# Optimization experiments

Hardware: AMD Instinct MI355X
Metric: run time of the kernel (lower is better)

## Reference

```python
import jax, jax.numpy as jnp
import numpy as np

N_FILTERS = 100
WINDOWS = (2, 3, 4, 5)
B, S, W, D = 64, 400, 16, 64
VOCAB, HID = 96, 128


def setup_inputs() -> dict:
    key = jax.random.key(0)
    ks = jax.random.split(key, 16)
    inp = {
        'char_idxs': jax.random.randint(ks[0], (B, S, W), 0, VOCAB),
        'char_vectors': jax.random.normal(ks[1], (VOCAB, D), jnp.float32),
        'filt2': jax.random.normal(ks[2], (N_FILTERS, 2 * D), jnp.float32) * 0.05,
        'filt3': jax.random.normal(ks[3], (N_FILTERS, 3 * D), jnp.float32) * 0.05,
        'filt4': jax.random.normal(ks[4], (N_FILTERS, 4 * D), jnp.float32) * 0.05,
        'filt5': jax.random.normal(ks[5], (N_FILTERS, 5 * D), jnp.float32) * 0.05,
        'w_proj': jax.random.normal(ks[6], (HID, 4 * N_FILTERS), jnp.float32) * 0.05,
        't_w0': jax.random.normal(ks[7], (HID, HID), jnp.float32) * 0.05,
        't_b0': jax.random.normal(ks[8], (HID,), jnp.float32) * 0.05,
        't_w1': jax.random.normal(ks[9], (HID, HID), jnp.float32) * 0.05,
        't_b1': jax.random.normal(ks[10], (HID,), jnp.float32) * 0.05,
        'g_w0': jax.random.normal(ks[11], (HID, HID), jnp.float32) * 0.05,
        'g_b0': jax.random.normal(ks[12], (HID,), jnp.float32) * 0.05,
        'g_w1': jax.random.normal(ks[13], (HID, HID), jnp.float32) * 0.05,
        'g_b1': jax.random.normal(ks[14], (HID,), jnp.float32) * 0.05,
    }
    return inp


def _conv_branch(embed, filt, w):
    # embed: [B, S, W, D]; filt: [100, w*D]
    b, s, wl, d = embed.shape
    L = wl - w + 1  # valid positions
    idx = jnp.arange(L)[:, None] + jnp.arange(w)  # [L, w]
    xw = embed[:, :, idx, :].reshape(b, s, L, w * d)  # [B,S,L,w*D]
    h = jnp.tanh(jnp.einsum('bslk,fk->bslf', xw, filt))  # [B,S,L,100]
    return h.max(axis=2)  # max-pool over all positions -> [B,S,100]


def reference(char_idxs, char_vectors, filt2, filt3, filt4, filt5, w_proj,
              t_w0, t_b0, t_w1, t_b1, g_w0, g_b0, g_w1, g_b1):
    embed = char_vectors[char_idxs]  # [B,S,W,D]
    outs = jnp.concatenate(
        [_conv_branch(embed, f, w) for f, w in zip((filt2, filt3, filt4, filt5), WINDOWS)],
        axis=-1)  # [B,S,400]
    x = outs @ w_proj.T  # no-bias linear -> [B,S,HID]
    # 2-layer highway: x = g*relu(Wt x + bt) + (1-g)*x, g = sigmoid(Wg x + bg)
    for tw, tb, gw, gb in ((t_w0, t_b0, g_w0, g_b0), (t_w1, t_b1, g_w1, g_b1)):
        g = jax.nn.sigmoid(x @ gw.T + gb)
        t = jax.nn.relu(x @ tw.T + tb)
        x = g * t + (1.0 - g) * x
    return x
```

## Files before the change

### kernel.cpp

```cpp
#include <hip/hip_runtime.h>

#define NT     25600
#define WCH    16
#define DIM    64
#define VOCAB  96
#define HID    128
#define KP     416
#define TOKB   64

typedef __attribute__((ext_vector_type(8))) _Float16 h8;
typedef __attribute__((ext_vector_type(4))) float f32x4;

__device__ __forceinline__ float tanh_fast(float m) {
  float t = fminf(fmaxf(m, -9.f), 9.f);
  float e = __builtin_amdgcn_exp2f(t * 2.885390082f);
  return 1.f - 2.f * __builtin_amdgcn_rcpf(e + 1.f);
}

__global__ __launch_bounds__(256) void k_prep(
    const float* __restrict__ cv,
    const float* __restrict__ f2, const float* __restrict__ f3,
    const float* __restrict__ f4, const float* __restrict__ f5,
    const float* __restrict__ wproj,
    const float* __restrict__ tw0, const float* __restrict__ gw0,
    const float* __restrict__ tw1, const float* __restrict__ gw1,
    _Float16* __restrict__ T2, _Float16* __restrict__ wprojP,
    _Float16* __restrict__ hw) {
  __shared__ float fS[100 * 65];
  __shared__ float cvS[8 * 65];
  const int tid = threadIdx.x;
  const int b = blockIdx.x;

  if (b < 168) {
    const int slot = b / 12, cg = b - slot * 12;
    int wi, j;
    if (slot < 2)      { wi = 0; j = slot; }
    else if (slot < 5) { wi = 1; j = slot - 2; }
    else if (slot < 9) { wi = 2; j = slot - 5; }
    else               { wi = 3; j = slot - 9; }
    const float* filt = (wi == 0) ? f2 : (wi == 1) ? f3 : (wi == 2) ? f4 : f5;
    const int rowlen = (wi + 2) * DIM;
    for (int idx = tid; idx < 100 * DIM; idx += 256) {
      int f = idx >> 6, d = idx & 63;
      fS[f * 65 + d] = filt[f * rowlen + j * DIM + d];
    }
    for (int idx = tid; idx < 8 * DIM; idx += 256) {
      int c = idx >> 6, d = idx & 63;
      cvS[c * 65 + d] = cv[(cg * 8 + c) * DIM + d];
    }
    __syncthreads();
    for (int idx = tid; idx < 8 * 104; idx += 256) {
      int cl = idx / 104, f = idx - cl * 104;
      float s = 0.f;
      if (f < 100) {
#pragma unroll 8
        for (int d = 0; d < DIM; ++d) s += cvS[cl * 65 + d] * fS[f * 65 + d];
      }
      T2[((size_t)(f >> 3) * 14 + slot) * 768 + (cg * 8 + cl) * 8 + (f & 7)] =
          (_Float16)s;
    }
  } else if (b < 232) {
    const int n = (b - 168) * 2 + (tid >> 7);
    for (int k = tid & 127; k < KP; k += 128) {
      int s8 = k >> 3;
      int wi = s8 / 13;
      int fl = (s8 - wi * 13) * 8 + (k & 7);
      wprojP[n * KP + k] =
          (fl < 100) ? (_Float16)wproj[n * 400 + wi * 100 + fl] : (_Float16)0.f;
    }
  } else {
    const int idx = (b - 232) * 256 + tid;
    const int which = idx >> 14, r = idx & 16383;
    const float* src = (which == 0) ? tw0 : (which == 1) ? gw0
                     : (which == 2) ? tw1 : gw1;
    hw[idx] = (_Float16)src[r];
  }
}

template<int WI>
__device__ __forceinline__ void conv_oct(const _Float16* __restrict__ Ts,
                                         const int* __restrict__ ch,
                                         _Float16* __restrict__ convA,
                                         int token, int o) {
  constexpr int W = WI + 2, L = 15 - WI;
  constexpr int SB = (WI == 0) ? 0 : (WI == 1) ? 2 : (WI == 2) ? 5 : 9;
  h8 m;
  {
    h8 s = *(const h8*)(Ts + SB * 768 + ch[0]);
#pragma unroll
    for (int j = 1; j < W; ++j) s += *(const h8*)(Ts + (SB + j) * 768 + ch[j]);
    m = s;
  }
#pragma unroll
  for (int l = 1; l < L; ++l) {
    h8 s = *(const h8*)(Ts + SB * 768 + ch[l]);
#pragma unroll
    for (int j = 1; j < W; ++j) s += *(const h8*)(Ts + (SB + j) * 768 + ch[l + j]);
    m = __builtin_elementwise_max(m, s);
  }
  h8 r;
#pragma unroll
  for (int i = 0; i < 8; ++i) r[i] = (_Float16)tanh_fast((float)m[i]);
  const int s8 = WI * 13 + o;
  *(h8*)(convA + (s8 * 64 + (token & 48) + ((token & 15) ^ (s8 & 15))) * 8) = r;
}

__global__ __launch_bounds__(256) void k_fused(
    const int* __restrict__ chars,
    const _Float16* __restrict__ T2,
    const _Float16* __restrict__ wprojP,
    const _Float16* __restrict__ hw,
    const float* __restrict__ tb0, const float* __restrict__ tb1,
    const float* __restrict__ gb0, const float* __restrict__ gb1,
    float* __restrict__ out) {
  __shared__ __align__(16) char lds[78848];
  _Float16* Ts    = (_Float16*)lds;
  _Float16* xA    = (_Float16*)lds;
  _Float16* convA = (_Float16*)(lds + 21504);
  int*      chS   = (int*)(lds + 21504 + 53248);

  const int tid = threadIdx.x;
  const int wave = tid >> 6, lane = tid & 63;
  const int m16 = lane & 15, quad = lane >> 4;
  const int tok0 = blockIdx.x * TOKB;
  const f32x4 zero = {0.f, 0.f, 0.f, 0.f};

#pragma unroll
  for (int k = 0; k < 4; ++k) {
    int idx = tid + k * 256;
    int t = idx >> 4, i = idx & 15;
    chS[i * 64 + t] = chars[(tok0 + t) * WCH + i] * 8;
  }
  __syncthreads();

  const int token = tid & 63;
  int ch[WCH];
#pragma unroll
  for (int i = 0; i < WCH; ++i) ch[i] = chS[i * 64 + token];

  for (int o = 0; o < 13; ++o) {
    if (o) __syncthreads();
    const _Float16* src = T2 + (size_t)o * 10752;
    for (int r = tid; r < 1344; r += 256)
      *(h8*)(Ts + r * 8) = *(const h8*)(src + r * 8);
    __syncthreads();
    switch ((wave + o) & 3) {
      case 0: conv_oct<0>(Ts, ch, convA, token, o); break;
      case 1: conv_oct<1>(Ts, ch, convA, token, o); break;
      case 2: conv_oct<2>(Ts, ch, convA, token, o); break;
      default: conv_oct<3>(Ts, ch, convA, token, o); break;
    }
  }
  __syncthreads();

  const int hcA = wave * 16 + m16;
  const int hcB = hcA + 64;
  f32x4 xp[4][2];
#pragma unroll
  for (int mt = 0; mt < 4; ++mt) { xp[mt][0] = zero; xp[mt][1] = zero; }

  for (int ks = 0; ks < 13; ++ks) {
    const int s8 = ks * 4 + quad;
    h8 b0 = *(const h8*)(wprojP + (size_t)hcA * KP + s8 * 8);
    h8 b1 = *(const h8*)(wprojP + (size_t)hcB * KP + s8 * 8);
#pragma unroll
    for (int mt = 0; mt < 4; ++mt) {
      h8 a = *(const h8*)(convA + (s8 * 64 + mt * 16 + (m16 ^ (s8 & 15))) * 8);
      xp[mt][0] = __builtin_amdgcn_mfma_f32_16x16x32_f16(a, b0, xp[mt][0], 0, 0, 0);
      xp[mt][1] = __builtin_amdgcn_mfma_f32_16x16x32_f16(a, b1, xp[mt][1], 0, 0, 0);
    }
  }

#pragma unroll
  for (int mt = 0; mt < 4; ++mt)
#pragma unroll
    for (int nt = 0; nt < 2; ++nt) {
      int col = nt * 64 + hcA;
#pragma unroll
      for (int r = 0; r < 4; ++r)
        xA[(col >> 3) * 512 + (mt * 16 + quad * 4 + r) * 8 + (col & 7)] =
            (_Float16)xp[mt][nt][r];
    }
  __syncthreads();

#pragma unroll
  for (int layer = 0; layer < 2; ++layer) {
    const _Float16* tw = hw + (layer ? 2 : 0) * HID * HID;
    const _Float16* gw = hw + (layer ? 3 : 1) * HID * HID;
    const float* tbv = layer ? tb1 : tb0;
    const float* gbv = layer ? gb1 : gb0;
    float btA = tbv[hcA], bgA = gbv[hcA];
    float btB = tbv[hcB], bgB = gbv[hcB];

    f32x4 at[4][2], ag[4][2];
#pragma unroll
    for (int mt = 0; mt < 4; ++mt) {
      at[mt][0] = zero; at[mt][1] = zero;
      ag[mt][0] = zero; ag[mt][1] = zero;
    }
#pragma unroll
    for (int ks = 0; ks < 4; ++ks) {
      const int ko = ks * 32 + quad * 8;
      h8 bt0 = *(const h8*)(tw + (size_t)hcA * HID + ko);
      h8 bt1 = *(const h8*)(tw + (size_t)hcB * HID + ko);
      h8 bg0 = *(const h8*)(gw + (size_t)hcA * HID + ko);
      h8 bg1 = *(const h8*)(gw + (size_t)hcB * HID + ko);
#pragma unroll
      for (int mt = 0; mt < 4; ++mt) {
        h8 a = *(const h8*)(xA + (ks * 4 + quad) * 512 + (mt * 16 + m16) * 8);
        at[mt][0] = __builtin_amdgcn_mfma_f32_16x16x32_f16(a, bt0, at[mt][0], 0, 0, 0);
        at[mt][1] = __builtin_amdgcn_mfma_f32_16x16x32_f16(a, bt1, at[mt][1], 0, 0, 0);
        ag[mt][0] = __builtin_amdgcn_mfma_f32_16x16x32_f16(a, bg0, ag[mt][0], 0, 0, 0);
        ag[mt][1] = __builtin_amdgcn_mfma_f32_16x16x32_f16(a, bg1, ag[mt][1], 0, 0, 0);
      }
    }
    __syncthreads();

#pragma unroll
    for (int mt = 0; mt < 4; ++mt)
#pragma unroll
      for (int nt = 0; nt < 2; ++nt) {
        float bt = nt ? btB : btA, bg = nt ? bgB : bgA;
        int col = nt * 64 + hcA;
#pragma unroll
        for (int r = 0; r < 4; ++r) {
          float g = 1.f / (1.f + __builtin_amdgcn_exp2f(
                               -(ag[mt][nt][r] + bg) * 1.442695041f));
          float tt = fmaxf(at[mt][nt][r] + bt, 0.f);
          float xn = g * tt + (1.f - g) * xp[mt][nt][r];
          xp[mt][nt][r] = xn;
          int row = mt * 16 + quad * 4 + r;
          if (layer == 0)
            xA[(col >> 3) * 512 + row * 8 + (col & 7)] = (_Float16)xn;
          else
            out[(size_t)(tok0 + row) * HID + col] = xn;
        }
      }
    if (layer == 0) __syncthreads();
  }
}

extern "C" void kernel_launch(void* const* d_in, const int* in_sizes, int n_in,
                              void* d_out, int out_size, void* d_ws, size_t ws_size,
                              hipStream_t stream) {
  (void)in_sizes; (void)n_in; (void)out_size; (void)ws_size;
  const int* chars = (const int*)d_in[0];
  const float* cv  = (const float*)d_in[1];
  const float* f2  = (const float*)d_in[2];
  const float* f3  = (const float*)d_in[3];
  const float* f4  = (const float*)d_in[4];
  const float* f5  = (const float*)d_in[5];
  const float* wpj = (const float*)d_in[6];
  const float* tw0 = (const float*)d_in[7];
  const float* tb0 = (const float*)d_in[8];
  const float* tw1 = (const float*)d_in[9];
  const float* tb1 = (const float*)d_in[10];
  const float* gw0 = (const float*)d_in[11];
  const float* gb0 = (const float*)d_in[12];
  const float* gw1 = (const float*)d_in[13];
  const float* gb1 = (const float*)d_in[14];
  float* out = (float*)d_out;

  char* ws = (char*)d_ws;
  _Float16* T2     = (_Float16*)ws;
  _Float16* wprojP = (_Float16*)(ws + 279552);
  _Float16* hw     = (_Float16*)(ws + 279552 + 106496);

  k_prep<<<488, 256, 0, stream>>>(cv, f2, f3, f4, f5, wpj, tw0, gw0, tw1, gw1,
                                  T2, wprojP, hw);
  k_fused<<<NT / TOKB, 256, 0, stream>>>(chars, T2, wprojP, hw,
                                         tb0, tb1, gb0, gb1, out);
}
```

Before: 175.4 us.

## Split conv-to-projection into two passes to shrink LDS and raise occupancy

The 13 conv octets are processed in two passes (7 then 6). The projection MFMA accumulation runs after each pass, so the convA staging buffer only needs room for 28 groups instead of 52. The char-index LDS staging is replaced with direct vectorized global loads per lane, and the XOR swizzle on convA is dropped. LDS per block falls from about 77KB to 49KB, which should allow more resident blocks per CU. The cost is extra barriers, and the unswizzled convA layout may bring back LDS bank conflicts.

```diff
diff --git a/kernel.cpp b/kernel.cpp
--- a/kernel.cpp
+++ b/kernel.cpp
@@ -10,6 +10,7 @@
 
 typedef __attribute__((ext_vector_type(8))) _Float16 h8;
 typedef __attribute__((ext_vector_type(4))) float f32x4;
+typedef __attribute__((ext_vector_type(4))) int i32x4;
 
 __device__ __forceinline__ float tanh_fast(float m) {
   float t = fminf(fmaxf(m, -9.f), 9.f);
@@ -81,7 +82,7 @@
 __device__ __forceinline__ void conv_oct(const _Float16* __restrict__ Ts,
                                          const int* __restrict__ ch,
                                          _Float16* __restrict__ convA,
-                                         int token, int o) {
+                                         int lane, int ls8) {
   constexpr int W = WI + 2, L = 15 - WI;
   constexpr int SB = (WI == 0) ? 0 : (WI == 1) ? 2 : (WI == 2) ? 5 : 9;
   h8 m;
@@ -101,8 +102,7 @@
   h8 r;
 #pragma unroll
   for (int i = 0; i < 8; ++i) r[i] = (_Float16)tanh_fast((float)m[i]);
-  const int s8 = WI * 13 + o;
-  *(h8*)(convA + (s8 * 64 + (token & 48) + ((token & 15) ^ (s8 & 15))) * 8) = r;
+  *(h8*)(convA + (ls8 * 64 + lane) * 8) = r;
 }
 
 __global__ __launch_bounds__(256) void k_fused(
@@ -113,11 +113,10 @@
     const float* __restrict__ tb0, const float* __restrict__ tb1,
     const float* __restrict__ gb0, const float* __restrict__ gb1,
     float* __restrict__ out) {
-  __shared__ __align__(16) char lds[78848];
+  __shared__ __align__(16) char lds[50176];
   _Float16* Ts    = (_Float16*)lds;
   _Float16* xA    = (_Float16*)lds;
   _Float16* convA = (_Float16*)(lds + 21504);
-  int*      chS   = (int*)(lds + 21504 + 53248);
 
   const int tid = threadIdx.x;
   const int wave = tid >> 6, lane = tid & 63;
@@ -125,33 +124,16 @@
   const int tok0 = blockIdx.x * TOKB;
   const f32x4 zero = {0.f, 0.f, 0.f, 0.f};
 
-#pragma unroll
-  for (int k = 0; k < 4; ++k) {
-    int idx = tid + k * 256;
-    int t = idx >> 4, i = idx & 15;
-    chS[i * 64 + t] = chars[(tok0 + t) * WCH + i] * 8;
-  }
-  __syncthreads();
-
-  const int token = tid & 63;
   int ch[WCH];
-#pragma unroll
-  for (int i = 0; i < WCH; ++i) ch[i] = chS[i * 64 + token];
-
-  for (int o = 0; o < 13; ++o) {
-    if (o) __syncthreads();
-    const _Float16* src = T2 + (size_t)o * 10752;
-    for (int r = tid; r < 1344; r += 256)
-      *(h8*)(Ts + r * 8) = *(const h8*)(src + r * 8);
-    __syncthreads();
-    switch ((wave + o) & 3) {
-      case 0: conv_oct<0>(Ts, ch, convA, token, o); break;
-      case 1: conv_oct<1>(Ts, ch, convA, token, o); break;
-      case 2: conv_oct<2>(Ts, ch, convA, token, o); break;
-      default: conv_oct<3>(Ts, ch, convA, token, o); break;
-    }
-  }
-  __syncthreads();
+  {
+    const i32x4* cp = (const i32x4*)(chars + (size_t)(tok0 + lane) * WCH);
+#pragma unroll
+    for (int q = 0; q < 4; ++q) {
+      i32x4 v = cp[q];
+#pragma unroll
+      for (int i = 0; i < 4; ++i) ch[q * 4 + i] = v[i] * 8;
+    }
+  }
 
   const int hcA = wave * 16 + m16;
   const int hcB = hcA + 64;
@@ -159,18 +141,44 @@
 #pragma unroll
   for (int mt = 0; mt < 4; ++mt) { xp[mt][0] = zero; xp[mt][1] = zero; }
 
-  for (int ks = 0; ks < 13; ++ks) {
-    const int s8 = ks * 4 + quad;
-    h8 b0 = *(const h8*)(wprojP + (size_t)hcA * KP + s8 * 8);
-    h8 b1 = *(const h8*)(wprojP + (size_t)hcB * KP + s8 * 8);
-#pragma unroll
-    for (int mt = 0; mt < 4; ++mt) {
-      h8 a = *(const h8*)(convA + (s8 * 64 + mt * 16 + (m16 ^ (s8 & 15))) * 8);
-      xp[mt][0] = __builtin_amdgcn_mfma_f32_16x16x32_f16(a, b0, xp[mt][0], 0, 0, 0);
-      xp[mt][1] = __builtin_amdgcn_mfma_f32_16x16x32_f16(a, b1, xp[mt][1], 0, 0, 0);
-    }
-  }
-
+#pragma unroll
+  for (int pass = 0; pass < 2; ++pass) {
+    const int obeg = pass ? 7 : 0, oend = pass ? 13 : 7;
+    for (int o = obeg; o < oend; ++o) {
+      __syncthreads();
+      const _Float16* src = T2 + (size_t)o * 10752;
+      for (int r = tid; r < 1344; r += 256)
+        *(h8*)(Ts + r * 8) = *(const h8*)(src + r * 8);
+      __syncthreads();
+      const int win = (wave + o) & 3;
+      const int ls8 = pass ? (win * 6 + o - 7) : (win * 7 + o);
+      switch (win) {
+        case 0: conv_oct<0>(Ts, ch, convA, lane, ls8); break;
+        case 1: conv_oct<1>(Ts, ch, convA, lane, ls8); break;
+        case 2: conv_oct<2>(Ts, ch, convA, lane, ls8); break;
+        default: conv_oct<3>(Ts, ch, convA, lane, ls8); break;
+      }
+    }
+    __syncthreads();
+    const int ng = pass ? 6 : 7;
+    const int per = pass ? 6 : 7;
+    const int ob = pass ? 7 : 0;
+    for (int ks = 0; ks < ng; ++ks) {
+      const int g = ks * 4 + quad;
+      const int win = g / per;
+      const int s8 = win * 13 + (g - win * per) + ob;
+      h8 b0 = *(const h8*)(wprojP + (size_t)hcA * KP + s8 * 8);
+      h8 b1 = *(const h8*)(wprojP + (size_t)hcB * KP + s8 * 8);
+#pragma unroll
+      for (int mt = 0; mt < 4; ++mt) {
+        h8 a = *(const h8*)(convA + (g * 64 + mt * 16 + m16) * 8);
+        xp[mt][0] = __builtin_amdgcn_mfma_f32_16x16x32_f16(a, b0, xp[mt][0], 0, 0, 0);
+        xp[mt][1] = __builtin_amdgcn_mfma_f32_16x16x32_f16(a, b1, xp[mt][1], 0, 0, 0);
+      }
+    }
+  }
+
+  __syncthreads();
 #pragma unroll
   for (int mt = 0; mt < 4; ++mt)
 #pragma unroll
```

Result: no change. 178.7 us (+1.9%).

## Read conv tables from global directly, widen block to 8 waves

Applied to the files above, without the earlier changes.

Removes the per-octet staging of the conv lookup tables into LDS, along with its 13 block-wide barriers. Each wave now gathers straight from the global/L2-resident table, and a static load-balanced split of filter octets is spread across 8 waves instead of 4. The projection and highway GEMMs are repartitioned so each wave owns 16 output columns, and char indices are read with vector loads. LDS use drops, which may raise occupancy. The cost is that the scattered gathers now hit the cache hierarchy instead of LDS, and the convA swizzle is removed, which could introduce bank conflicts.

```diff
diff --git a/kernel.cpp b/kernel.cpp
--- a/kernel.cpp
+++ b/kernel.cpp
@@ -10,6 +10,7 @@
 
 typedef __attribute__((ext_vector_type(8))) _Float16 h8;
 typedef __attribute__((ext_vector_type(4))) float f32x4;
+typedef __attribute__((ext_vector_type(4))) int i32x4;
 
 __device__ __forceinline__ float tanh_fast(float m) {
   float t = fminf(fmaxf(m, -9.f), 9.f);
@@ -78,34 +79,35 @@
 }
 
 template<int WI>
-__device__ __forceinline__ void conv_oct(const _Float16* __restrict__ Ts,
-                                         const int* __restrict__ ch,
-                                         _Float16* __restrict__ convA,
-                                         int token, int o) {
+__device__ __forceinline__ void conv_g(const _Float16* __restrict__ T2,
+                                       const int* __restrict__ ch,
+                                       _Float16* __restrict__ convA,
+                                       int lane, int o) {
   constexpr int W = WI + 2, L = 15 - WI;
   constexpr int SB = (WI == 0) ? 0 : (WI == 1) ? 2 : (WI == 2) ? 5 : 9;
+  const _Float16* Tb = T2 + ((size_t)o * 14 + SB) * 768;
   h8 m;
   {
-    h8 s = *(const h8*)(Ts + SB * 768 + ch[0]);
-#pragma unroll
-    for (int j = 1; j < W; ++j) s += *(const h8*)(Ts + (SB + j) * 768 + ch[j]);
+    h8 s = *(const h8*)(Tb + ch[0]);
+#pragma unroll
+    for (int j = 1; j < W; ++j) s += *(const h8*)(Tb + j * 768 + ch[j]);
     m = s;
   }
 #pragma unroll
   for (int l = 1; l < L; ++l) {
-    h8 s = *(const h8*)(Ts + SB * 768 + ch[l]);
-#pragma unroll
-    for (int j = 1; j < W; ++j) s += *(const h8*)(Ts + (SB + j) * 768 + ch[l + j]);
+    h8 s = *(const h8*)(Tb + ch[l]);
+#pragma unroll
+    for (int j = 1; j < W; ++j) s += *(const h8*)(Tb + j * 768 + ch[l + j]);
     m = __builtin_elementwise_max(m, s);
   }
   h8 r;
 #pragma unroll
   for (int i = 0; i < 8; ++i) r[i] = (_Float16)tanh_fast((float)m[i]);
   const int s8 = WI * 13 + o;
-  *(h8*)(convA + (s8 * 64 + (token & 48) + ((token & 15) ^ (s8 & 15))) * 8) = r;
-}
-
-__global__ __launch_bounds__(256) void k_fused(
+  *(h8*)(convA + (s8 * 64 + lane) * 8) = r;
+}
+
+__global__ __launch_bounds__(512) void k_fused(
     const int* __restrict__ chars,
     const _Float16* __restrict__ T2,
     const _Float16* __restrict__ wprojP,
@@ -113,11 +115,9 @@
     const float* __restrict__ tb0, const float* __restrict__ tb1,
     const float* __restrict__ gb0, const float* __restrict__ gb1,
     float* __restrict__ out) {
-  __shared__ __align__(16) char lds[78848];
-  _Float16* Ts    = (_Float16*)lds;
+  __shared__ __align__(16) char lds[53248];
+  _Float16* convA = (_Float16*)lds;
   _Float16* xA    = (_Float16*)lds;
-  _Float16* convA = (_Float16*)(lds + 21504);
-  int*      chS   = (int*)(lds + 21504 + 53248);
 
   const int tid = threadIdx.x;
   const int wave = tid >> 6, lane = tid & 63;
@@ -125,62 +125,54 @@
   const int tok0 = blockIdx.x * TOKB;
   const f32x4 zero = {0.f, 0.f, 0.f, 0.f};
 
-#pragma unroll
-  for (int k = 0; k < 4; ++k) {
-    int idx = tid + k * 256;
-    int t = idx >> 4, i = idx & 15;
-    chS[i * 64 + t] = chars[(tok0 + t) * WCH + i] * 8;
+  int ch[WCH];
+  {
+    const i32x4* cp = (const i32x4*)(chars + (size_t)(tok0 + lane) * WCH);
+#pragma unroll
+    for (int q = 0; q < 4; ++q) {
+      i32x4 v = cp[q];
+#pragma unroll
+      for (int i = 0; i < 4; ++i) ch[q * 4 + i] = v[i] * 8;
+    }
+  }
+
+  switch (wave) {
+    case 0: for (int o = 0;  o < 5;  ++o) conv_g<3>(T2, ch, convA, lane, o); break;
+    case 1: for (int o = 5;  o < 10; ++o) conv_g<3>(T2, ch, convA, lane, o); break;
+    case 2: for (int o = 10; o < 13; ++o) conv_g<3>(T2, ch, convA, lane, o);
+            for (int o = 0;  o < 2;  ++o) conv_g<2>(T2, ch, convA, lane, o); break;
+    case 3: for (int o = 2;  o < 8;  ++o) conv_g<2>(T2, ch, convA, lane, o); break;
+    case 4: for (int o = 8;  o < 13; ++o) conv_g<2>(T2, ch, convA, lane, o);
+            conv_g<0>(T2, ch, convA, lane, 0); break;
+    case 5: for (int o = 0;  o < 7;  ++o) conv_g<1>(T2, ch, convA, lane, o); break;
+    case 6: for (int o = 7;  o < 13; ++o) conv_g<1>(T2, ch, convA, lane, o);
+            conv_g<0>(T2, ch, convA, lane, 1); break;
+    default: for (int o = 2; o < 13; ++o) conv_g<0>(T2, ch, convA, lane, o); break;
   }
   __syncthreads();
 
-  const int token = tid & 63;
-  int ch[WCH];
-#pragma unroll
-  for (int i = 0; i < WCH; ++i) ch[i] = chS[i * 64 + token];
-
-  for (int o = 0; o < 13; ++o) {
-    if (o) __syncthreads();
-    const _Float16* src = T2 + (size_t)o * 10752;
-    for (int r = tid; r < 1344; r += 256)
-      *(h8*)(Ts + r * 8) = *(const h8*)(src + r * 8);
-    __syncthreads();
-    switch ((wave + o) & 3) {
-      case 0: conv_oct<0>(Ts, ch, convA, token, o); break;
-      case 1: conv_oct<1>(Ts, ch, convA, token, o); break;
-      case 2: conv_oct<2>(Ts, ch, convA, token, o); break;
-      default: conv_oct<3>(Ts, ch, convA, token, o); break;
-    }
-  }
-  __syncthreads();
-
-  const int hcA = wave * 16 + m16;
-  const int hcB = hcA + 64;
-  f32x4 xp[4][2];
-#pragma unroll
-  for (int mt = 0; mt < 4; ++mt) { xp[mt][0] = zero; xp[mt][1] = zero; }
+  const int hc = wave * 16 + m16;
+  f32x4 xp[4];
+#pragma unroll
+  for (int mt = 0; mt < 4; ++mt) xp[mt] = zero;
 
   for (int ks = 0; ks < 13; ++ks) {
     const int s8 = ks * 4 + quad;
-    h8 b0 = *(const h8*)(wprojP + (size_t)hcA * KP + s8 * 8);
-    h8 b1 = *(const h8*)(wprojP + (size_t)hcB * KP + s8 * 8);
+    h8 b = *(const h8*)(wprojP + (size_t)hc * KP + s8 * 8);
 #pragma unroll
     for (int mt = 0; mt < 4; ++mt) {
-      h8 a = *(const h8*)(convA + (s8 * 64 + mt * 16 + (m16 ^ (s8 & 15))) * 8);
-      xp[mt][0] = __builtin_amdgcn_mfma_f32_16x16x32_f16(a, b0, xp[mt][0], 0, 0, 0);
-      xp[mt][1] = __builtin_amdgcn_mfma_f32_16x16x32_f16(a, b1, xp[mt][1], 0, 0, 0);
-    }
-  }
+      h8 a = *(const h8*)(convA + (s8 * 64 + mt * 16 + m16) * 8);
+      xp[mt] = __builtin_amdgcn_mfma_f32_16x16x32_f16(a, b, xp[mt], 0, 0, 0);
+    }
+  }
+  __syncthreads();
 
 #pragma unroll
   for (int mt = 0; mt < 4; ++mt)
 #pragma unroll
-    for (int nt = 0; nt < 2; ++nt) {
-      int col = nt * 64 + hcA;
-#pragma unroll
-      for (int r = 0; r < 4; ++r)
-        xA[(col >> 3) * 512 + (mt * 16 + quad * 4 + r) * 8 + (col & 7)] =
-            (_Float16)xp[mt][nt][r];
-    }
+    for (int r = 0; r < 4; ++r)
+      xA[(hc >> 3) * 512 + (mt * 16 + quad * 4 + r) * 8 + (hc & 7)] =
+          (_Float16)xp[mt][r];
   __syncthreads();
 
 #pragma unroll
@@ -189,29 +181,22 @@
     const _Float16* gw = hw + (layer ? 3 : 1) * HID * HID;
     const float* tbv = layer ? tb1 : tb0;
     const float* gbv = layer ? gb1 : gb0;
-    float btA = tbv[hcA], bgA = gbv[hcA];
-    float btB = tbv[hcB], bgB = gbv[hcB];
-
-    f32x4 at[4][2], ag[4][2];
-#pragma unroll
-    for (int mt = 0; mt < 4; ++mt) {
-      at[mt][0] = zero; at[mt][1] = zero;
-      ag[mt][0] = zero; ag[mt][1] = zero;
-    }
+    float bt = tbv[hc], bg = gbv[hc];
+
+    f32x4 at[4], ag[4];
+#pragma unroll
+    for (int mt = 0; mt < 4; ++mt) { at[mt] = zero; ag[mt] = zero; }
+
 #pragma unroll
     for (int ks = 0; ks < 4; ++ks) {
       const int ko = ks * 32 + quad * 8;
-      h8 bt0 = *(const h8*)(tw + (size_t)hcA * HID + ko);
-      h8 bt1 = *(const h8*)(tw + (size_t)hcB * HID + ko);
-      h8 bg0 = *(const h8*)(gw + (size_t)hcA * HID + ko);
-      h8 bg1 = *(const h8*)(gw + (size_t)hcB * HID + ko);
+      h8 btw = *(const h8*)(tw + (size_t)hc * HID + ko);
+      h8 bgw = *(const h8*)(gw + (size_t)hc * HID + ko);
 #pragma unroll
       for (int mt = 0; mt < 4; ++mt) {
         h8 a = *(const h8*)(xA + (ks * 4 + quad) * 512 + (mt * 16 + m16) * 8);
-        at[mt][0] = __builtin_amdgcn_mfma_f32_16x16x32_f16(a, bt0, at[mt][0], 0, 0, 0);
-        at[mt][1] = __builtin_amdgcn_mfma_f32_16x16x32_f16(a, bt1, at[mt][1], 0, 0, 0);
-        ag[mt][0] = __builtin_amdgcn_mfma_f32_16x16x32_f16(a, bg0, ag[mt][0], 0, 0, 0);
-        ag[mt][1] = __builtin_amdgcn_mfma_f32_16x16x32_f16(a, bg1, ag[mt][1], 0, 0, 0);
+        at[mt] = __builtin_amdgcn_mfma_f32_16x16x32_f16(a, btw, at[mt], 0, 0, 0);
+        ag[mt] = __builtin_amdgcn_mfma_f32_16x16x32_f16(a, bgw, ag[mt], 0, 0, 0);
       }
     }
     __syncthreads();
@@ -219,22 +204,17 @@
 #pragma unroll
     for (int mt = 0; mt < 4; ++mt)
 #pragma unroll
-      for (int nt = 0; nt < 2; ++nt) {
-        float bt = nt ? btB : btA, bg = nt ? bgB : bgA;
-        int col = nt * 64 + hcA;
-#pragma unroll
-        for (int r = 0; r < 4; ++r) {
-          float g = 1.f / (1.f + __builtin_amdgcn_exp2f(
-                               -(ag[mt][nt][r] + bg) * 1.442695041f));
-          float tt = fmaxf(at[mt][nt][r] + bt, 0.f);
-          float xn = g * tt + (1.f - g) * xp[mt][nt][r];
-          xp[mt][nt][r] = xn;
-          int row = mt * 16 + quad * 4 + r;
-          if (layer == 0)
-            xA[(col >> 3) * 512 + row * 8 + (col & 7)] = (_Float16)xn;
-          else
-            out[(size_t)(tok0 + row) * HID + col] = xn;
-        }
+      for (int r = 0; r < 4; ++r) {
+        float g = 1.f / (1.f + __builtin_amdgcn_exp2f(
+                             -(ag[mt][r] + bg) * 1.442695041f));
+        float tt = fmaxf(at[mt][r] + bt, 0.f);
+        float xn = g * tt + (1.f - g) * xp[mt][r];
+        xp[mt][r] = xn;
+        int row = mt * 16 + quad * 4 + r;
+        if (layer == 0)
+          xA[(hc >> 3) * 512 + row * 8 + (hc & 7)] = (_Float16)xn;
+        else
+          out[(size_t)(tok0 + row) * HID + hc] = xn;
       }
     if (layer == 0) __syncthreads();
   }
@@ -268,6 +248,6 @@
 
   k_prep<<<488, 256, 0, stream>>>(cv, f2, f3, f4, f5, wpj, tw0, gw0, tw1, gw1,
                                   T2, wprojP, hw);
-  k_fused<<<NT / TOKB, 256, 0, stream>>>(chars, T2, wprojP, hw,
+  k_fused<<<NT / TOKB, 512, 0, stream>>>(chars, T2, wprojP, hw,
                                          tb0, tb1, gb0, gb1, out);
 }
```

Result: slower. 180.1 us (+2.7%).
